# Performance work log

Hardware: AMD Instinct MI355X
Metric: run time of the kernel (lower is better)

The kernel has to match this reference:

```python
import jax, jax.numpy as jnp
import numpy as np
import math

N_HEADS = 16
D_MODEL = 1024
D_K = D_MODEL // N_HEADS
NEG_INF = -1e9
LN_EPS = 1e-5


def setup_inputs() -> dict:
    key = jax.random.key(0)
    ks = jax.random.split(key, 10)
    B, S = 8, 1024
    x = jax.random.normal(ks[0], (B, S, D_MODEL), dtype=jnp.float32)
    mask = jnp.ones((B, S, 1), dtype=jnp.float32)
    s = 1.0 / math.sqrt(D_MODEL)
    # per-head Linear weights, torch layout [out, in] stacked over heads
    wq = jax.random.uniform(ks[1], (N_HEADS, D_K, D_MODEL), jnp.float32, -s, s)
    bq = jax.random.uniform(ks[2], (N_HEADS, D_K), jnp.float32, -s, s)
    wk = jax.random.uniform(ks[3], (N_HEADS, D_K, D_MODEL), jnp.float32, -s, s)
    bk = jax.random.uniform(ks[4], (N_HEADS, D_K), jnp.float32, -s, s)
    wv = jax.random.uniform(ks[5], (N_HEADS, D_K, D_MODEL), jnp.float32, -s, s)
    bv = jax.random.uniform(ks[6], (N_HEADS, D_K), jnp.float32, -s, s)
    w_out = jax.random.uniform(ks[7], (D_MODEL, D_MODEL), jnp.float32, -s, s)
    b_out = jax.random.uniform(ks[8], (D_MODEL,), jnp.float32, -s, s)
    return {"x": x, "mask": mask, "wq": wq, "bq": bq, "wk": wk, "bk": bk,
            "wv": wv, "bv": bv, "w_out": w_out, "b_out": b_out}


def _masked_softmax(scores, mask2d, axis):
    # mask2d: [B,S,S] broadcast over heads; zero entries get -1e9 before softmax
    masked = jnp.where(mask2d[:, None, :, :] > 0, scores, NEG_INF)
    return jax.nn.softmax(masked, axis=axis)


def reference(x, mask, wq, bq, wk, bk, wv, bv, w_out, b_out):
    B, S, D = x.shape
    # layer_norm over last dim, no affine params (F.layer_norm defaults)
    mu = jnp.mean(x, axis=-1, keepdims=True)
    var = jnp.var(x, axis=-1, keepdims=True)
    xn = (x - mu) * jax.lax.rsqrt(var + LN_EPS)
    # batched per-head projections: [B,H,S,d_k]
    q = jnp.einsum('bsd,hkd->bhsk', xn, wq) + bq[None, :, None, :]
    k = jnp.einsum('bsd,hkd->bhsk', xn, wk) + bk[None, :, None, :]
    v = jnp.einsum('bsd,hkd->bhsk', xn, wv) + bv[None, :, None, :]
    scores = jnp.einsum('bhsk,bhtk->bhst', q, k) / math.sqrt(D_K)
    mask2d = jnp.einsum('bsi,bti->bst', mask, mask)  # [B,S,S]
    # double masked softmax: first over query dim (torch dim=1), then key dim (dim=2)
    attn = _masked_softmax(scores, mask2d, axis=2)
    attn = _masked_softmax(attn, mask2d, axis=3)
    heads = jnp.einsum('bhst,bhtk->bshk', attn, v)  # [B,S,H,d_v]
    heads = heads.reshape(B, S, D)
    return heads @ w_out.T + b_out + x
```

## Files before the change

kernel.cpp:

```cpp
#include <hip/hip_runtime.h>


typedef unsigned short ushort_t;
typedef unsigned short us4 __attribute__((ext_vector_type(4)));
typedef unsigned short us8 __attribute__((ext_vector_type(8)));
typedef __bf16 bf16x8 __attribute__((ext_vector_type(8)));
typedef float f32x4 __attribute__((ext_vector_type(4)));

#define QSCALE 0.18033688011112042f
#define LOG2E 1.4426950408889634f
#define MNEG (-1.0e9f)
#define EXP2(x) __builtin_amdgcn_exp2f(x)

__device__ __forceinline__ ushort_t f2bf(float f) {
    unsigned int u = __float_as_uint(f);
    return (ushort_t)((u + 0x7fffu + ((u >> 16) & 1u)) >> 16);
}

#define GLDS(gp, lp)                                                        \
    __builtin_amdgcn_global_load_lds(                                       \
        (const __attribute__((address_space(1))) unsigned int*)(gp),        \
        (__attribute__((address_space(3))) unsigned int*)(lp), 16, 0, 0)

#define MFMA(a, b, c) __builtin_amdgcn_mfma_f32_16x16x32_bf16((a), (b), (c), 0, 0, 0)

__global__ __launch_bounds__(256) void ln_kernel(const float* __restrict__ x,
                                                 ushort_t* __restrict__ xn) {
    int row = blockIdx.x, tid = threadIdx.x;
    float4 v = ((const float4*)(x + (size_t)row * 1024))[tid];
    float s = v.x + v.y + v.z + v.w;
    __shared__ float red[8];
    for (int o = 32; o > 0; o >>= 1) s += __shfl_down(s, o);
    int wave = tid >> 6, lane = tid & 63;
    if (lane == 0) red[wave] = s;
    __syncthreads();
    float mu = (red[0] + red[1] + red[2] + red[3]) * (1.0f / 1024.0f);
    float d0 = v.x - mu, d1 = v.y - mu, d2 = v.z - mu, d3 = v.w - mu;
    float q = d0 * d0 + d1 * d1 + d2 * d2 + d3 * d3;
    for (int o = 32; o > 0; o >>= 1) q += __shfl_down(q, o);
    if (lane == 0) red[wave + 4] = q;
    __syncthreads();
    float var = (red[4] + red[5] + red[6] + red[7]) * (1.0f / 1024.0f);
    float rs = rsqrtf(var + 1e-5f);
    us4 ov;
    ov[0] = f2bf(d0 * rs); ov[1] = f2bf(d1 * rs);
    ov[2] = f2bf(d2 * rs); ov[3] = f2bf(d3 * rs);
    ((us4*)(xn + (size_t)row * 1024))[tid] = ov;
}

__global__ __launch_bounds__(256) void wconv(const float* __restrict__ src,
                                             ushort_t* __restrict__ dst) {
    size_t i = ((size_t)blockIdx.x * 256 + threadIdx.x) * 4;
    float4 f = *(const float4*)(src + i);
    us4 o;
    o[0] = f2bf(f.x); o[1] = f2bf(f.y); o[2] = f2bf(f.z); o[3] = f2bf(f.w);
    *(us4*)(dst + i) = o;
}

__global__ __launch_bounds__(256) void tailcopy(const us8* __restrict__ src,
                                                us8* __restrict__ dst) {
    size_t i = (size_t)blockIdx.x * 256 + threadIdx.x;
    dst[i] = src[i];
}

template <int BMODE, int OMODE>
__global__ __launch_bounds__(256) void gemm_mfma(
    const ushort_t* __restrict__ A, const void* __restrict__ Bq,
    const void* __restrict__ Bk, const void* __restrict__ Bv,
    const float* __restrict__ biasq, const float* __restrict__ biask,
    const float* __restrict__ biasv, ushort_t* __restrict__ oq,
    ushort_t* __restrict__ ok, ushort_t* __restrict__ ovt,
    float* __restrict__ ofp, const float* __restrict__ resx, int batched,
    int r0base, int aoff) {
    __shared__ ushort_t As[128 * 32] __attribute__((aligned(16)));
    __shared__ ushort_t Bs[128 * 32] __attribute__((aligned(16)));
    int tid = threadIdx.x, w = tid >> 6, lane = tid & 63;
    int quad = lane >> 4, l15 = lane & 15;
    int wm = w & 1, wn = w >> 1;
    int csw = (quad ^ ((l15 >> 1) & 3)) * 8;
    int n0 = blockIdx.x * 128;
    int r0 = r0base + blockIdx.y * 128;
    int wsel = blockIdx.z;
    const void* Bp = (wsel == 0) ? Bq : (wsel == 1) ? Bk : Bv;
    const float* biasp = (wsel == 0) ? biasq : (wsel == 1) ? biask : biasv;
    const float qscale = (OMODE == 0 && wsel == 0) ? QSCALE : 1.0f;

    f32x4 acc[4][4];
#pragma unroll
    for (int i = 0; i < 4; i++)
#pragma unroll
        for (int j = 0; j < 4; j++) acc[i][j] = (f32x4){0.f, 0.f, 0.f, 0.f};

    for (int k0 = 0; k0 < 1024; k0 += 32) {
        __syncthreads();
#pragma unroll
        for (int ii = 0; ii < 2; ii++) {
            int li = (w * 2 + ii) * 64 + lane;
            int row = li >> 2, kc = li & 3;
            int sk = kc ^ ((row >> 1) & 3);
            GLDS(A + (size_t)(r0 + row - aoff) * 1024 + k0 + sk * 8,
                 &As[(w * 2 + ii) * 512]);
        }
        if (BMODE == 0) {
#pragma unroll
            for (int ii = 0; ii < 2; ii++) {
                int li = (w * 2 + ii) * 64 + lane;
                int row = li >> 2, kc = li & 3;
                int sk = kc ^ ((row >> 1) & 3);
                GLDS((const ushort_t*)Bp + (size_t)(n0 + row) * 1024 + k0 + sk * 8,
                     &Bs[(w * 2 + ii) * 512]);
            }
        } else {
            int row = tid >> 1, half = tid & 1;
            int sw = (row >> 1) & 3;
            const float* gb =
                (const float*)Bp + (size_t)(n0 + row) * 1024 + k0 + half * 16;
            float4 f0 = *(const float4*)gb;
            float4 f1 = *(const float4*)(gb + 4);
            float4 f2 = *(const float4*)(gb + 8);
            float4 f3 = *(const float4*)(gb + 12);
            us8 p0, p1;
            p0[0] = f2bf(f0.x); p0[1] = f2bf(f0.y); p0[2] = f2bf(f0.z); p0[3] = f2bf(f0.w);
            p0[4] = f2bf(f1.x); p0[5] = f2bf(f1.y); p0[6] = f2bf(f1.z); p0[7] = f2bf(f1.w);
            p1[0] = f2bf(f2.x); p1[1] = f2bf(f2.y); p1[2] = f2bf(f2.z); p1[3] = f2bf(f2.w);
            p1[4] = f2bf(f3.x); p1[5] = f2bf(f3.y); p1[6] = f2bf(f3.z); p1[7] = f2bf(f3.w);
            *(us8*)&Bs[row * 32 + ((half * 2) ^ sw) * 8] = p0;
            *(us8*)&Bs[row * 32 + ((half * 2 + 1) ^ sw) * 8] = p1;
        }
        __syncthreads();
        bf16x8 a[4], b[4];
#pragma unroll
        for (int i = 0; i < 4; i++)
            a[i] = *(const bf16x8*)&As[(wm * 64 + i * 16 + l15) * 32 + csw];
#pragma unroll
        for (int j = 0; j < 4; j++)
            b[j] = *(const bf16x8*)&Bs[(wn * 64 + j * 16 + l15) * 32 + csw];
#pragma unroll
        for (int i = 0; i < 4; i++)
#pragma unroll
            for (int j = 0; j < 4; j++) acc[i][j] = MFMA(a[i], b[j], acc[i][j]);
    }
#pragma unroll
    for (int j = 0; j < 4; j++) {
        int n = n0 + wn * 64 + j * 16 + l15;
        float bj = biasp[n];
        if (OMODE == 0) {
            int h = n >> 6, kk = n & 63;
#pragma unroll
            for (int i = 0; i < 4; i++) {
#pragma unroll
                for (int v = 0; v < 4; v++) {
                    int r = r0 + wm * 64 + i * 16 + quad * 4 + v;
                    int bb = batched ? (r >> 10) : 0;
                    int s = r & 1023;
                    ushort_t val = f2bf((acc[i][j][v] + bj) * qscale);
                    if (wsel < 2) {
                        ushort_t* op = (wsel == 0) ? oq : ok;
                        op[((size_t)(bb * 16 + h) * 1024 + s) * 64 + kk] = val;
                    } else {
                        ovt[((size_t)(bb * 16 + h) * 64 + kk) * 1024 + s] = val;
                    }
                }
            }
        } else {
#pragma unroll
            for (int i = 0; i < 4; i++) {
#pragma unroll
                for (int v = 0; v < 4; v++) {
                    int r = r0 + wm * 64 + i * 16 + quad * 4 + v;
                    size_t idx = (size_t)r * 1024 + n;
                    ofp[idx] = acc[i][j][v] + bj + resx[idx];
                }
            }
        }
    }
}

__global__ __launch_bounds__(256) void colstats_mfma(
    const ushort_t* __restrict__ qb, const ushort_t* __restrict__ kb,
    const float* __restrict__ mask, int moff, float* __restrict__ colsum) {
    __shared__ ushort_t Ks[4096] __attribute__((aligned(16)));
    __shared__ ushort_t Qs[4096] __attribute__((aligned(16)));
    __shared__ float mk[64], mq[64], red[4][64];
    int tid = threadIdx.x, w = tid >> 6, lane = tid & 63;
    int quad = lane >> 4, l15 = lane & 15;
    int csw = (quad ^ ((l15 >> 1) & 3)) * 8;
    int by = blockIdx.y;
    size_t qoff = (size_t)by * 65536;
    int coff = by * 1024;
    int mb = moff + (by >> 4) * 1024;
    int t0 = blockIdx.x * 64;
#pragma unroll
    for (int ii = 0; ii < 2; ii++) {
        int qq = w * 2 + ii, half = qq >> 2, sub = qq & 3;
        int li = sub * 64 + lane, row = li >> 2, seg = li & 3;
        int sk = seg ^ ((row >> 1) & 3);
        GLDS(kb + qoff + (size_t)(t0 + row) * 64 + half * 32 + sk * 8,
             &Ks[half * 2048 + sub * 512]);
    }
    if (tid < 64) mk[tid] = mask[mb + t0 + tid];
    __syncthreads();
    bf16x8 kf0[4], kf1[4];
#pragma unroll
    for (int j = 0; j < 4; j++) {
        kf0[j] = *(const bf16x8*)&Ks[(j * 16 + l15) * 32 + csw];
        kf1[j] = *(const bf16x8*)&Ks[2048 + (j * 16 + l15) * 32 + csw];
    }
    float amk[4];
#pragma unroll
    for (int j = 0; j < 4; j++) amk[j] = (mk[j * 16 + l15] > 0.f) ? 0.f : MNEG;
    float colacc[4] = {0.f, 0.f, 0.f, 0.f};
    for (int s0 = 0; s0 < 1024; s0 += 64) {
        __syncthreads();
#pragma unroll
        for (int ii = 0; ii < 2; ii++) {
            int qq = w * 2 + ii, half = qq >> 2, sub = qq & 3;
            int li = sub * 64 + lane, row = li >> 2, seg = li & 3;
            int sk = seg ^ ((row >> 1) & 3);
            GLDS(qb + qoff + (size_t)(s0 + row) * 64 + half * 32 + sk * 8,
                 &Qs[half * 2048 + sub * 512]);
        }
        if (tid < 64) mq[tid] = mask[mb + s0 + tid];
        __syncthreads();
        float amq[4];
#pragma unroll
        for (int v = 0; v < 4; v++)
            amq[v] = (mq[w * 16 + quad * 4 + v] > 0.f) ? 0.f : MNEG;
        bf16x8 a0 = *(const bf16x8*)&Qs[(w * 16 + l15) * 32 + csw];
        bf16x8 a1 = *(const bf16x8*)&Qs[2048 + (w * 16 + l15) * 32 + csw];
#pragma unroll
        for (int j = 0; j < 4; j++) {
            f32x4 sc = (f32x4){0.f, 0.f, 0.f, 0.f};
            sc = MFMA(a0, kf0[j], sc);
            sc = MFMA(a1, kf1[j], sc);
#pragma unroll
            for (int v = 0; v < 4; v++)
                colacc[j] += EXP2(sc[v] + amq[v] + amk[j]);
        }
    }
#pragma unroll
    for (int j = 0; j < 4; j++) {
        float vv = colacc[j];
        vv += __shfl_down(vv, 32);
        vv += __shfl_down(vv, 16);
        if (quad == 0) red[w][j * 16 + l15] = vv;
    }
    __syncthreads();
    if (tid < 64)
        colsum[coff + t0 + tid] = red[0][tid] + red[1][tid] + red[2][tid] + red[3][tid];
}

__global__ __launch_bounds__(256) void pv_mfma(
    const ushort_t* __restrict__ qb, const ushort_t* __restrict__ kb,
    const ushort_t* __restrict__ vtb, const float* __restrict__ mask, int moff,
    const float* __restrict__ colsum, ushort_t* __restrict__ H, int hbase) {
    __shared__ ushort_t Qs[4096] __attribute__((aligned(16)));
    __shared__ ushort_t Ks[4096] __attribute__((aligned(16)));
    __shared__ ushort_t Vt[4096] __attribute__((aligned(16)));
    __shared__ ushort_t E[64 * 72] __attribute__((aligned(16)));
    __shared__ float mk[64], mq[64], ics[64];
    int tid = threadIdx.x, w = tid >> 6, lane = tid & 63;
    int quad = lane >> 4, l15 = lane & 15;
    int csw = (quad ^ ((l15 >> 1) & 3)) * 8;
    int by = blockIdx.y;
    size_t qoff = (size_t)by * 65536;
    int coff = by * 1024;
    int mb = moff + (by >> 4) * 1024;
    int h = by & 15;
    int s0 = blockIdx.x * 64;
#pragma unroll
    for (int ii = 0; ii < 2; ii++) {
        int qq = w * 2 + ii, half = qq >> 2, sub = qq & 3;
        int li = sub * 64 + lane, row = li >> 2, seg = li & 3;
        int sk = seg ^ ((row >> 1) & 3);
        GLDS(qb + qoff + (size_t)(s0 + row) * 64 + half * 32 + sk * 8,
             &Qs[half * 2048 + sub * 512]);
    }
    if (tid < 64) mq[tid] = mask[mb + s0 + tid];
    __syncthreads();
    bf16x8 a0 = *(const bf16x8*)&Qs[(w * 16 + l15) * 32 + csw];
    bf16x8 a1 = *(const bf16x8*)&Qs[2048 + (w * 16 + l15) * 32 + csw];
    float amq[4];
#pragma unroll
    for (int v = 0; v < 4; v++)
        amq[v] = (mq[w * 16 + quad * 4 + v] > 0.f) ? 0.f : MNEG;
    bf16x8 ones;
#pragma unroll
    for (int e = 0; e < 8; e++) ones[e] = (__bf16)1.0f;
    f32x4 acc_o[4], acc_rs = (f32x4){0.f, 0.f, 0.f, 0.f};
#pragma unroll
    for (int j = 0; j < 4; j++) acc_o[j] = (f32x4){0.f, 0.f, 0.f, 0.f};
    for (int t0 = 0; t0 < 1024; t0 += 64) {
        __syncthreads();
#pragma unroll
        for (int ii = 0; ii < 2; ii++) {
            int qq = w * 2 + ii, half = qq >> 2, sub = qq & 3;
            int li = sub * 64 + lane, row = li >> 2, seg = li & 3;
            int sk = seg ^ ((row >> 1) & 3);
            GLDS(kb + qoff + (size_t)(t0 + row) * 64 + half * 32 + sk * 8,
                 &Ks[half * 2048 + sub * 512]);
            GLDS(vtb + qoff + (size_t)row * 1024 + t0 + half * 32 + sk * 8,
                 &Vt[half * 2048 + sub * 512]);
        }
        if (tid < 64) {
            mk[tid] = mask[mb + t0 + tid];
            float cs = colsum[coff + t0 + tid];
            ics[tid] = (cs > 0.f) ? LOG2E / cs : 0.f;
        }
        __syncthreads();
#pragma unroll
        for (int j = 0; j < 4; j++) {
            bf16x8 b0 = *(const bf16x8*)&Ks[(j * 16 + l15) * 32 + csw];
            bf16x8 b1 = *(const bf16x8*)&Ks[2048 + (j * 16 + l15) * 32 + csw];
            f32x4 sc = (f32x4){0.f, 0.f, 0.f, 0.f};
            sc = MFMA(a0, b0, sc);
            sc = MFMA(a1, b1, sc);
            int tcol = j * 16 + l15;
            float icv = ics[tcol];
            float aj = (mk[tcol] > 0.f) ? 0.f : MNEG;
#pragma unroll
            for (int v = 0; v < 4; v++) {
                float e1 = EXP2(sc[v]);
                float e2 = EXP2(fmaf(e1, icv, amq[v] + aj));
                int sl = w * 16 + quad * 4 + v;
                E[sl * 72 + tcol] = (ushort_t)(__float_as_uint(e2) >> 16);
            }
        }
        bf16x8 ea0 = *(const bf16x8*)&E[(w * 16 + l15) * 72 + quad * 8];
        bf16x8 ea1 = *(const bf16x8*)&E[(w * 16 + l15) * 72 + 32 + quad * 8];
#pragma unroll
        for (int j = 0; j < 4; j++) {
            bf16x8 b0 = *(const bf16x8*)&Vt[(j * 16 + l15) * 32 + csw];
            bf16x8 b1 = *(const bf16x8*)&Vt[2048 + (j * 16 + l15) * 32 + csw];
            acc_o[j] = MFMA(ea0, b0, acc_o[j]);
            acc_o[j] = MFMA(ea1, b1, acc_o[j]);
        }
        acc_rs = MFMA(ea0, ones, acc_rs);
        acc_rs = MFMA(ea1, ones, acc_rs);
    }
#pragma unroll
    for (int v = 0; v < 4; v++) {
        int sl = w * 16 + quad * 4 + v;
        int hr = hbase + (by >> 4) * 1024 + s0 + sl;
        ushort_t* hp = H + (size_t)hr * 1024;
        float inv = 1.0f / fmaxf(acc_rs[v], 1e-30f);
#pragma unroll
        for (int j = 0; j < 4; j++)
            hp[h * 64 + j * 16 + l15] = f2bf(acc_o[j][v] * inv);
    }
}

extern "C" void kernel_launch(void* const* d_in, const int* in_sizes, int n_in,
                              void* d_out, int out_size, void* d_ws, size_t ws_size,
                              hipStream_t stream) {
    const float* x     = (const float*)d_in[0];
    const float* mask  = (const float*)d_in[1];
    const float* wq    = (const float*)d_in[2];
    const float* bq    = (const float*)d_in[3];
    const float* wk    = (const float*)d_in[4];
    const float* bk    = (const float*)d_in[5];
    const float* wv    = (const float*)d_in[6];
    const float* bv    = (const float*)d_in[7];
    const float* w_out = (const float*)d_in[8];
    const float* b_out = (const float*)d_in[9];
    float* outp = (float*)d_out;

    const size_t MB = 1024 * 1024;
    ushort_t* xn = (ushort_t*)d_out;
    ushort_t* H  = (ushort_t*)d_out + 8 * MB;
    char* ws = (char*)d_ws;

    ln_kernel<<<dim3(8192), 256, 0, stream>>>(x, xn);

    if (ws_size >= 58 * MB) {
        ushort_t* qb  = (ushort_t*)ws;
        ushort_t* kb  = (ushort_t*)(ws + 16 * MB);
        ushort_t* vtb = (ushort_t*)(ws + 32 * MB);
        float* csum   = (float*)(ws + 48 * MB);
        ushort_t* wqb = (ushort_t*)(ws + 49 * MB);
        ushort_t* wkb = (ushort_t*)(ws + 51 * MB);
        ushort_t* wvb = (ushort_t*)(ws + 53 * MB);
        ushort_t* wob = (ushort_t*)(ws + 55 * MB);
        float* ofull  = (float*)ws;
        wconv<<<dim3(1024), 256, 0, stream>>>(wq, wqb);
        wconv<<<dim3(1024), 256, 0, stream>>>(wk, wkb);
        wconv<<<dim3(1024), 256, 0, stream>>>(wv, wvb);
        wconv<<<dim3(1024), 256, 0, stream>>>(w_out, wob);
        gemm_mfma<0, 0><<<dim3(8, 64, 3), 256, 0, stream>>>(
            xn, wqb, wkb, wvb, bq, bk, bv, qb, kb, vtb, nullptr, nullptr, 1, 0, 0);
        colstats_mfma<<<dim3(16, 128), 256, 0, stream>>>(qb, kb, mask, 0, csum);
        pv_mfma<<<dim3(16, 128), 256, 0, stream>>>(qb, kb, vtb, mask, 0, csum, H, 0);
        gemm_mfma<0, 1><<<dim3(8, 64), 256, 0, stream>>>(
            H, wob, wob, wob, b_out, b_out, b_out, nullptr, nullptr, nullptr,
            ofull, x, 0, 0, 0);
        hipMemcpyAsync(d_out, ofull, 32 * MB, hipMemcpyDeviceToDevice, stream);
    } else {
        ushort_t* qb  = (ushort_t*)ws;
        ushort_t* kb  = (ushort_t*)(ws + 2 * MB);
        ushort_t* vtb = (ushort_t*)(ws + 4 * MB);
        float* csum   = (float*)(ws + 6 * MB);
        ushort_t* hcopy = (ushort_t*)ws;
        const int casc[6][2] = {{0, 32},   {4096, 16}, {6144, 8},
                                {7168, 4}, {7680, 2},  {7936, 1}};
        for (int g = 0; g < 8; g++) {
            gemm_mfma<1, 0><<<dim3(8, 8, 3), 256, 0, stream>>>(
                xn + (size_t)g * MB, wq, wk, wv, bq, bk, bv, qb, kb, vtb,
                nullptr, nullptr, 0, 0, 0);
            colstats_mfma<<<dim3(16, 16), 256, 0, stream>>>(qb, kb, mask,
                                                            g * 1024, csum);
            pv_mfma<<<dim3(16, 16), 256, 0, stream>>>(qb, kb, vtb, mask,
                                                      g * 1024, csum, H, g * 1024);
        }
        tailcopy<<<dim3(64), 256, 0, stream>>>((const us8*)(H + (size_t)8064 * 1024),
                                               (us8*)hcopy);
        for (int i = 0; i < 6; i++)
            gemm_mfma<1, 1><<<dim3(8, casc[i][1]), 256, 0, stream>>>(
                H, w_out, w_out, w_out, b_out, b_out, b_out, nullptr, nullptr,
                nullptr, outp, x, 0, casc[i][0], 0);
        gemm_mfma<1, 1><<<dim3(8, 1), 256, 0, stream>>>(
            hcopy, w_out, w_out, w_out, b_out, b_out, b_out, nullptr, nullptr,
            nullptr, outp, x, 0, 8064, 8064);
    }
}
```

Before: 354.5 us.

## Double-buffer LDS tiles in GEMM, column-stats and attention kernels

Adds ping-pong shared-memory buffers to the projection GEMM, the column-softmax statistics kernel and the attention kernel. The next K/V, Q or A/B tile is prefetched with async global-to-LDS loads while the current tile is consumed by MFMAs. This leaves one barrier per iteration instead of two. The aim is to hide global load latency behind compute, at the cost of roughly doubled LDS use per block, which could lower occupancy.

```diff
diff --git a/kernel.cpp b/kernel.cpp
--- a/kernel.cpp
+++ b/kernel.cpp
@@ -72,8 +72,8 @@
     ushort_t* __restrict__ ok, ushort_t* __restrict__ ovt,
     float* __restrict__ ofp, const float* __restrict__ resx, int batched,
     int r0base, int aoff) {
-    __shared__ ushort_t As[128 * 32] __attribute__((aligned(16)));
-    __shared__ ushort_t Bs[128 * 32] __attribute__((aligned(16)));
+    __shared__ ushort_t As[2][128 * 32] __attribute__((aligned(16)));
+    __shared__ ushort_t Bs[2][128 * 32] __attribute__((aligned(16)));
     int tid = threadIdx.x, w = tid >> 6, lane = tid & 63;
     int quad = lane >> 4, l15 = lane & 15;
     int wm = w & 1, wn = w >> 1;
@@ -85,21 +85,14 @@
     const float* biasp = (wsel == 0) ? biasq : (wsel == 1) ? biask : biasv;
     const float qscale = (OMODE == 0 && wsel == 0) ? QSCALE : 1.0f;
 
-    f32x4 acc[4][4];
-#pragma unroll
-    for (int i = 0; i < 4; i++)
-#pragma unroll
-        for (int j = 0; j < 4; j++) acc[i][j] = (f32x4){0.f, 0.f, 0.f, 0.f};
-
-    for (int k0 = 0; k0 < 1024; k0 += 32) {
-        __syncthreads();
+    auto stage = [&](int buf, int k0) {
 #pragma unroll
         for (int ii = 0; ii < 2; ii++) {
             int li = (w * 2 + ii) * 64 + lane;
             int row = li >> 2, kc = li & 3;
             int sk = kc ^ ((row >> 1) & 3);
             GLDS(A + (size_t)(r0 + row - aoff) * 1024 + k0 + sk * 8,
-                 &As[(w * 2 + ii) * 512]);
+                 &As[buf][(w * 2 + ii) * 512]);
         }
         if (BMODE == 0) {
 #pragma unroll
@@ -108,7 +101,7 @@
                 int row = li >> 2, kc = li & 3;
                 int sk = kc ^ ((row >> 1) & 3);
                 GLDS((const ushort_t*)Bp + (size_t)(n0 + row) * 1024 + k0 + sk * 8,
-                     &Bs[(w * 2 + ii) * 512]);
+                     &Bs[buf][(w * 2 + ii) * 512]);
             }
         } else {
             int row = tid >> 1, half = tid & 1;
@@ -124,21 +117,35 @@
             p0[4] = f2bf(f1.x); p0[5] = f2bf(f1.y); p0[6] = f2bf(f1.z); p0[7] = f2bf(f1.w);
             p1[0] = f2bf(f2.x); p1[1] = f2bf(f2.y); p1[2] = f2bf(f2.z); p1[3] = f2bf(f2.w);
             p1[4] = f2bf(f3.x); p1[5] = f2bf(f3.y); p1[6] = f2bf(f3.z); p1[7] = f2bf(f3.w);
-            *(us8*)&Bs[row * 32 + ((half * 2) ^ sw) * 8] = p0;
-            *(us8*)&Bs[row * 32 + ((half * 2 + 1) ^ sw) * 8] = p1;
-        }
+            *(us8*)&Bs[buf][row * 32 + ((half * 2) ^ sw) * 8] = p0;
+            *(us8*)&Bs[buf][row * 32 + ((half * 2 + 1) ^ sw) * 8] = p1;
+        }
+    };
+
+    f32x4 acc[4][4];
+    stage(0, 0);
+#pragma unroll
+    for (int i = 0; i < 4; i++)
+#pragma unroll
+        for (int j = 0; j < 4; j++) acc[i][j] = (f32x4){0.f, 0.f, 0.f, 0.f};
+    __syncthreads();
+
+    int cur = 0;
+    for (int k0 = 0; k0 < 1024; k0 += 32) {
+        if (k0 + 32 < 1024) stage(cur ^ 1, k0 + 32);
+        bf16x8 a[4], b[4];
+#pragma unroll
+        for (int i = 0; i < 4; i++)
+            a[i] = *(const bf16x8*)&As[cur][(wm * 64 + i * 16 + l15) * 32 + csw];
+#pragma unroll
+        for (int j = 0; j < 4; j++)
+            b[j] = *(const bf16x8*)&Bs[cur][(wn * 64 + j * 16 + l15) * 32 + csw];
+#pragma unroll
+        for (int i = 0; i < 4; i++)
+#pragma unroll
+            for (int j = 0; j < 4; j++) acc[i][j] = MFMA(a[i], b[j], acc[i][j]);
         __syncthreads();
-        bf16x8 a[4], b[4];
-#pragma unroll
-        for (int i = 0; i < 4; i++)
-            a[i] = *(const bf16x8*)&As[(wm * 64 + i * 16 + l15) * 32 + csw];
-#pragma unroll
-        for (int j = 0; j < 4; j++)
-            b[j] = *(const bf16x8*)&Bs[(wn * 64 + j * 16 + l15) * 32 + csw];
-#pragma unroll
-        for (int i = 0; i < 4; i++)
-#pragma unroll
-            for (int j = 0; j < 4; j++) acc[i][j] = MFMA(a[i], b[j], acc[i][j]);
+        cur ^= 1;
     }
 #pragma unroll
     for (int j = 0; j < 4; j++) {
@@ -180,8 +187,8 @@
     const ushort_t* __restrict__ qb, const ushort_t* __restrict__ kb,
     const float* __restrict__ mask, int moff, float* __restrict__ colsum) {
     __shared__ ushort_t Ks[4096] __attribute__((aligned(16)));
-    __shared__ ushort_t Qs[4096] __attribute__((aligned(16)));
-    __shared__ float mk[64], mq[64], red[4][64];
+    __shared__ ushort_t Qs[2][4096] __attribute__((aligned(16)));
+    __shared__ float mk[64], mq[2][64], red[4][64];
     int tid = threadIdx.x, w = tid >> 6, lane = tid & 63;
     int quad = lane >> 4, l15 = lane & 15;
     int csw = (quad ^ ((l15 >> 1) & 3)) * 8;
@@ -190,6 +197,18 @@
     int coff = by * 1024;
     int mb = moff + (by >> 4) * 1024;
     int t0 = blockIdx.x * 64;
+
+    auto stageQ = [&](int buf, int ss) {
+#pragma unroll
+        for (int ii = 0; ii < 2; ii++) {
+            int qq = w * 2 + ii, half = qq >> 2, sub = qq & 3;
+            int li = sub * 64 + lane, row = li >> 2, seg = li & 3;
+            int sk = seg ^ ((row >> 1) & 3);
+            GLDS(qb + qoff + (size_t)(ss + row) * 64 + half * 32 + sk * 8,
+                 &Qs[buf][half * 2048 + sub * 512]);
+        }
+    };
+
 #pragma unroll
     for (int ii = 0; ii < 2; ii++) {
         int qq = w * 2 + ii, half = qq >> 2, sub = qq & 3;
@@ -199,6 +218,8 @@
              &Ks[half * 2048 + sub * 512]);
     }
     if (tid < 64) mk[tid] = mask[mb + t0 + tid];
+    stageQ(0, 0);
+    if (tid < 64) mq[0][tid] = mask[mb + tid];
     __syncthreads();
     bf16x8 kf0[4], kf1[4];
 #pragma unroll
@@ -210,24 +231,18 @@
 #pragma unroll
     for (int j = 0; j < 4; j++) amk[j] = (mk[j * 16 + l15] > 0.f) ? 0.f : MNEG;
     float colacc[4] = {0.f, 0.f, 0.f, 0.f};
+    int cur = 0;
     for (int s0 = 0; s0 < 1024; s0 += 64) {
-        __syncthreads();
-#pragma unroll
-        for (int ii = 0; ii < 2; ii++) {
-            int qq = w * 2 + ii, half = qq >> 2, sub = qq & 3;
-            int li = sub * 64 + lane, row = li >> 2, seg = li & 3;
-            int sk = seg ^ ((row >> 1) & 3);
-            GLDS(qb + qoff + (size_t)(s0 + row) * 64 + half * 32 + sk * 8,
-                 &Qs[half * 2048 + sub * 512]);
-        }
-        if (tid < 64) mq[tid] = mask[mb + s0 + tid];
-        __syncthreads();
+        if (s0 + 64 < 1024) {
+            stageQ(cur ^ 1, s0 + 64);
+            if (tid < 64) mq[cur ^ 1][tid] = mask[mb + s0 + 64 + tid];
+        }
         float amq[4];
 #pragma unroll
         for (int v = 0; v < 4; v++)
-            amq[v] = (mq[w * 16 + quad * 4 + v] > 0.f) ? 0.f : MNEG;
-        bf16x8 a0 = *(const bf16x8*)&Qs[(w * 16 + l15) * 32 + csw];
-        bf16x8 a1 = *(const bf16x8*)&Qs[2048 + (w * 16 + l15) * 32 + csw];
+            amq[v] = (mq[cur][w * 16 + quad * 4 + v] > 0.f) ? 0.f : MNEG;
+        bf16x8 a0 = *(const bf16x8*)&Qs[cur][(w * 16 + l15) * 32 + csw];
+        bf16x8 a1 = *(const bf16x8*)&Qs[cur][2048 + (w * 16 + l15) * 32 + csw];
 #pragma unroll
         for (int j = 0; j < 4; j++) {
             f32x4 sc = (f32x4){0.f, 0.f, 0.f, 0.f};
@@ -237,6 +252,8 @@
             for (int v = 0; v < 4; v++)
                 colacc[j] += EXP2(sc[v] + amq[v] + amk[j]);
         }
+        __syncthreads();
+        cur ^= 1;
     }
 #pragma unroll
     for (int j = 0; j < 4; j++) {
@@ -255,10 +272,10 @@
     const ushort_t* __restrict__ vtb, const float* __restrict__ mask, int moff,
     const float* __restrict__ colsum, ushort_t* __restrict__ H, int hbase) {
     __shared__ ushort_t Qs[4096] __attribute__((aligned(16)));
-    __shared__ ushort_t Ks[4096] __attribute__((aligned(16)));
-    __shared__ ushort_t Vt[4096] __attribute__((aligned(16)));
+    __shared__ ushort_t Ks[2][4096] __attribute__((aligned(16)));
+    __shared__ ushort_t Vt[2][4096] __attribute__((aligned(16)));
     __shared__ ushort_t E[64 * 72] __attribute__((aligned(16)));
-    __shared__ float mk[64], mq[64], ics[64];
+    __shared__ float mk[2][64], mq[64], ics[2][64];
     int tid = threadIdx.x, w = tid >> 6, lane = tid & 63;
     int quad = lane >> 4, l15 = lane & 15;
     int csw = (quad ^ ((l15 >> 1) & 3)) * 8;
@@ -268,6 +285,25 @@
     int mb = moff + (by >> 4) * 1024;
     int h = by & 15;
     int s0 = blockIdx.x * 64;
+
+    auto stageKV = [&](int buf, int tt) {
+#pragma unroll
+        for (int ii = 0; ii < 2; ii++) {
+            int qq = w * 2 + ii, half = qq >> 2, sub = qq & 3;
+            int li = sub * 64 + lane, row = li >> 2, seg = li & 3;
+            int sk = seg ^ ((row >> 1) & 3);
+            GLDS(kb + qoff + (size_t)(tt + row) * 64 + half * 32 + sk * 8,
+                 &Ks[buf][half * 2048 + sub * 512]);
+            GLDS(vtb + qoff + (size_t)row * 1024 + tt + half * 32 + sk * 8,
+                 &Vt[buf][half * 2048 + sub * 512]);
+        }
+        if (tid < 64) {
+            mk[buf][tid] = mask[mb + tt + tid];
+            float cs = colsum[coff + tt + tid];
+            ics[buf][tid] = (cs > 0.f) ? LOG2E / cs : 0.f;
+        }
+    };
+
 #pragma unroll
     for (int ii = 0; ii < 2; ii++) {
         int qq = w * 2 + ii, half = qq >> 2, sub = qq & 3;
@@ -277,6 +313,7 @@
              &Qs[half * 2048 + sub * 512]);
     }
     if (tid < 64) mq[tid] = mask[mb + s0 + tid];
+    stageKV(0, 0);
     __syncthreads();
     bf16x8 a0 = *(const bf16x8*)&Qs[(w * 16 + l15) * 32 + csw];
     bf16x8 a1 = *(const bf16x8*)&Qs[2048 + (w * 16 + l15) * 32 + csw];
@@ -290,34 +327,19 @@
     f32x4 acc_o[4], acc_rs = (f32x4){0.f, 0.f, 0.f, 0.f};
 #pragma unroll
     for (int j = 0; j < 4; j++) acc_o[j] = (f32x4){0.f, 0.f, 0.f, 0.f};
+    int cur = 0;
     for (int t0 = 0; t0 < 1024; t0 += 64) {
-        __syncthreads();
-#pragma unroll
-        for (int ii = 0; ii < 2; ii++) {
-            int qq = w * 2 + ii, half = qq >> 2, sub = qq & 3;
-            int li = sub * 64 + lane, row = li >> 2, seg = li & 3;
-            int sk = seg ^ ((row >> 1) & 3);
-            GLDS(kb + qoff + (size_t)(t0 + row) * 64 + half * 32 + sk * 8,
-                 &Ks[half * 2048 + sub * 512]);
-            GLDS(vtb + qoff + (size_t)row * 1024 + t0 + half * 32 + sk * 8,
-                 &Vt[half * 2048 + sub * 512]);
-        }
-        if (tid < 64) {
-            mk[tid] = mask[mb + t0 + tid];
-            float cs = colsum[coff + t0 + tid];
-            ics[tid] = (cs > 0.f) ? LOG2E / cs : 0.f;
-        }
-        __syncthreads();
+        if (t0 + 64 < 1024) stageKV(cur ^ 1, t0 + 64);
 #pragma unroll
         for (int j = 0; j < 4; j++) {
-            bf16x8 b0 = *(const bf16x8*)&Ks[(j * 16 + l15) * 32 + csw];
-            bf16x8 b1 = *(const bf16x8*)&Ks[2048 + (j * 16 + l15) * 32 + csw];
+            bf16x8 b0 = *(const bf16x8*)&Ks[cur][(j * 16 + l15) * 32 + csw];
+            bf16x8 b1 = *(const bf16x8*)&Ks[cur][2048 + (j * 16 + l15) * 32 + csw];
             f32x4 sc = (f32x4){0.f, 0.f, 0.f, 0.f};
             sc = MFMA(a0, b0, sc);
             sc = MFMA(a1, b1, sc);
             int tcol = j * 16 + l15;
-            float icv = ics[tcol];
-            float aj = (mk[tcol] > 0.f) ? 0.f : MNEG;
+            float icv = ics[cur][tcol];
+            float aj = (mk[cur][tcol] > 0.f) ? 0.f : MNEG;
 #pragma unroll
             for (int v = 0; v < 4; v++) {
                 float e1 = EXP2(sc[v]);
@@ -330,13 +352,15 @@
         bf16x8 ea1 = *(const bf16x8*)&E[(w * 16 + l15) * 72 + 32 + quad * 8];
 #pragma unroll
         for (int j = 0; j < 4; j++) {
-            bf16x8 b0 = *(const bf16x8*)&Vt[(j * 16 + l15) * 32 + csw];
-            bf16x8 b1 = *(const bf16x8*)&Vt[2048 + (j * 16 + l15) * 32 + csw];
+            bf16x8 b0 = *(const bf16x8*)&Vt[cur][(j * 16 + l15) * 32 + csw];
+            bf16x8 b1 = *(const bf16x8*)&Vt[cur][2048 + (j * 16 + l15) * 32 + csw];
             acc_o[j] = MFMA(ea0, b0, acc_o[j]);
             acc_o[j] = MFMA(ea1, b1, acc_o[j]);
         }
         acc_rs = MFMA(ea0, ones, acc_rs);
         acc_rs = MFMA(ea1, ones, acc_rs);
+        __syncthreads();
+        cur ^= 1;
     }
 #pragma unroll
     for (int v = 0; v < 4; v++) {
```

New measurement: 382.1 us. +7.8%, slower.

## Double-buffer GEMM LDS tiles and remap workgroups across XCDs for L2 locality

Applied to the files above, without the earlier changes.

The GEMM main loop now uses two LDS buffers and issues the loads for the next K tile before running the MFMAs on the current one, with a single barrier per iteration. This is meant to overlap global-to-LDS traffic with compute. Separately, GEMM, colstats and pv kernels remap the linear workgroup id so that consecutive logical tiles land on the same XCD, improving L2 reuse of the shared K/V and weight tiles. LDS usage in the GEMM doubles, which may reduce occupancy.

```diff
diff --git a/kernel.cpp b/kernel.cpp
--- a/kernel.cpp
+++ b/kernel.cpp
@@ -15,6 +15,14 @@
 __device__ __forceinline__ ushort_t f2bf(float f) {
     unsigned int u = __float_as_uint(f);
     return (ushort_t)((u + 0x7fffu + ((u >> 16) & 1u)) >> 16);
+}
+
+__device__ __forceinline__ int xcd_remap() {
+    int nwg = gridDim.x * gridDim.y * gridDim.z;
+    int o = blockIdx.x + gridDim.x * (blockIdx.y + gridDim.y * blockIdx.z);
+    int q = nwg >> 3, r = nwg & 7;
+    int xcd = o & 7, i = o >> 3;
+    return (xcd < r ? xcd * (q + 1) : r * (q + 1) + (xcd - r) * q) + i;
 }
 
 #define GLDS(gp, lp)                                                        \
@@ -72,34 +80,30 @@
     ushort_t* __restrict__ ok, ushort_t* __restrict__ ovt,
     float* __restrict__ ofp, const float* __restrict__ resx, int batched,
     int r0base, int aoff) {
-    __shared__ ushort_t As[128 * 32] __attribute__((aligned(16)));
-    __shared__ ushort_t Bs[128 * 32] __attribute__((aligned(16)));
+    __shared__ ushort_t As[2][128 * 32] __attribute__((aligned(16)));
+    __shared__ ushort_t Bs[2][128 * 32] __attribute__((aligned(16)));
     int tid = threadIdx.x, w = tid >> 6, lane = tid & 63;
     int quad = lane >> 4, l15 = lane & 15;
     int wm = w & 1, wn = w >> 1;
     int csw = (quad ^ ((l15 >> 1) & 3)) * 8;
-    int n0 = blockIdx.x * 128;
-    int r0 = r0base + blockIdx.y * 128;
-    int wsel = blockIdx.z;
+    int wg = xcd_remap();
+    int gxz = gridDim.x * gridDim.z;
+    int wy = wg / gxz, wt = wg % gxz;
+    int n0 = (wt % gridDim.x) * 128;
+    int r0 = r0base + wy * 128;
+    int wsel = wt / gridDim.x;
     const void* Bp = (wsel == 0) ? Bq : (wsel == 1) ? Bk : Bv;
     const float* biasp = (wsel == 0) ? biasq : (wsel == 1) ? biask : biasv;
     const float qscale = (OMODE == 0 && wsel == 0) ? QSCALE : 1.0f;
 
-    f32x4 acc[4][4];
-#pragma unroll
-    for (int i = 0; i < 4; i++)
-#pragma unroll
-        for (int j = 0; j < 4; j++) acc[i][j] = (f32x4){0.f, 0.f, 0.f, 0.f};
-
-    for (int k0 = 0; k0 < 1024; k0 += 32) {
-        __syncthreads();
+    auto stage = [&](int buf, int k0) {
 #pragma unroll
         for (int ii = 0; ii < 2; ii++) {
             int li = (w * 2 + ii) * 64 + lane;
             int row = li >> 2, kc = li & 3;
             int sk = kc ^ ((row >> 1) & 3);
             GLDS(A + (size_t)(r0 + row - aoff) * 1024 + k0 + sk * 8,
-                 &As[(w * 2 + ii) * 512]);
+                 &As[buf][(w * 2 + ii) * 512]);
         }
         if (BMODE == 0) {
 #pragma unroll
@@ -108,7 +112,7 @@
                 int row = li >> 2, kc = li & 3;
                 int sk = kc ^ ((row >> 1) & 3);
                 GLDS((const ushort_t*)Bp + (size_t)(n0 + row) * 1024 + k0 + sk * 8,
-                     &Bs[(w * 2 + ii) * 512]);
+                     &Bs[buf][(w * 2 + ii) * 512]);
             }
         } else {
             int row = tid >> 1, half = tid & 1;
@@ -124,21 +128,35 @@
             p0[4] = f2bf(f1.x); p0[5] = f2bf(f1.y); p0[6] = f2bf(f1.z); p0[7] = f2bf(f1.w);
             p1[0] = f2bf(f2.x); p1[1] = f2bf(f2.y); p1[2] = f2bf(f2.z); p1[3] = f2bf(f2.w);
             p1[4] = f2bf(f3.x); p1[5] = f2bf(f3.y); p1[6] = f2bf(f3.z); p1[7] = f2bf(f3.w);
-            *(us8*)&Bs[row * 32 + ((half * 2) ^ sw) * 8] = p0;
-            *(us8*)&Bs[row * 32 + ((half * 2 + 1) ^ sw) * 8] = p1;
-        }
+            *(us8*)&Bs[buf][row * 32 + ((half * 2) ^ sw) * 8] = p0;
+            *(us8*)&Bs[buf][row * 32 + ((half * 2 + 1) ^ sw) * 8] = p1;
+        }
+    };
+
+    f32x4 acc[4][4];
+    stage(0, 0);
+#pragma unroll
+    for (int i = 0; i < 4; i++)
+#pragma unroll
+        for (int j = 0; j < 4; j++) acc[i][j] = (f32x4){0.f, 0.f, 0.f, 0.f};
+    __syncthreads();
+
+    int cur = 0;
+    for (int k0 = 0; k0 < 1024; k0 += 32) {
+        if (k0 + 32 < 1024) stage(cur ^ 1, k0 + 32);
+        bf16x8 a[4], b[4];
+#pragma unroll
+        for (int i = 0; i < 4; i++)
+            a[i] = *(const bf16x8*)&As[cur][(wm * 64 + i * 16 + l15) * 32 + csw];
+#pragma unroll
+        for (int j = 0; j < 4; j++)
+            b[j] = *(const bf16x8*)&Bs[cur][(wn * 64 + j * 16 + l15) * 32 + csw];
+#pragma unroll
+        for (int i = 0; i < 4; i++)
+#pragma unroll
+            for (int j = 0; j < 4; j++) acc[i][j] = MFMA(a[i], b[j], acc[i][j]);
         __syncthreads();
-        bf16x8 a[4], b[4];
-#pragma unroll
-        for (int i = 0; i < 4; i++)
-            a[i] = *(const bf16x8*)&As[(wm * 64 + i * 16 + l15) * 32 + csw];
-#pragma unroll
-        for (int j = 0; j < 4; j++)
-            b[j] = *(const bf16x8*)&Bs[(wn * 64 + j * 16 + l15) * 32 + csw];
-#pragma unroll
-        for (int i = 0; i < 4; i++)
-#pragma unroll
-            for (int j = 0; j < 4; j++) acc[i][j] = MFMA(a[i], b[j], acc[i][j]);
+        cur ^= 1;
     }
 #pragma unroll
     for (int j = 0; j < 4; j++) {
@@ -185,11 +203,12 @@
     int tid = threadIdx.x, w = tid >> 6, lane = tid & 63;
     int quad = lane >> 4, l15 = lane & 15;
     int csw = (quad ^ ((l15 >> 1) & 3)) * 8;
-    int by = blockIdx.y;
+    int wg = xcd_remap();
+    int by = wg / gridDim.x;
+    int t0 = (wg % gridDim.x) * 64;
     size_t qoff = (size_t)by * 65536;
     int coff = by * 1024;
     int mb = moff + (by >> 4) * 1024;
-    int t0 = blockIdx.x * 64;
 #pragma unroll
     for (int ii = 0; ii < 2; ii++) {
         int qq = w * 2 + ii, half = qq >> 2, sub = qq & 3;
@@ -262,12 +281,13 @@
     int tid = threadIdx.x, w = tid >> 6, lane = tid & 63;
     int quad = lane >> 4, l15 = lane & 15;
     int csw = (quad ^ ((l15 >> 1) & 3)) * 8;
-    int by = blockIdx.y;
+    int wg = xcd_remap();
+    int by = wg / gridDim.x;
+    int s0 = (wg % gridDim.x) * 64;
     size_t qoff = (size_t)by * 65536;
     int coff = by * 1024;
     int mb = moff + (by >> 4) * 1024;
     int h = by & 15;
-    int s0 = blockIdx.x * 64;
 #pragma unroll
     for (int ii = 0; ii < 2; ii++) {
         int qq = w * 2 + ii, half = qq >> 2, sub = qq & 3;
```

After: 360.0 us. Within noise of the previous version (+1.5%).
